# Optimization experiments

Hardware: AMD Instinct MI355X
Metric: run time of the kernel (lower is better)

Reference implementation:

```python
import jax, jax.numpy as jnp
import numpy as np

B, S, H, HD = 2, 2048, 16, 128
HID = H * HD            # 2048
FF = 4 * HID            # 8192
ROT = int(HD * 0.25)    # 32 rotary dims (rotary_pct=0.25)
EPS = 1e-5
ROPE_BASE = 10000.0


def _layernorm(x, g, b):
    mu = jnp.mean(x, axis=-1, keepdims=True)
    var = jnp.mean(jnp.square(x - mu), axis=-1, keepdims=True)
    return (x - mu) * jax.lax.rsqrt(var + EPS) * g + b


def _rope_cos_sin(seq_len, dim, dtype):
    inv_freq = 1.0 / (ROPE_BASE ** (np.arange(0, dim, 2, dtype=np.float32) / dim))
    t = np.arange(seq_len, dtype=np.float32)
    freqs = np.outer(t, inv_freq)              # [S, dim/2]
    emb = np.concatenate([freqs, freqs], -1)   # [S, dim]
    return jnp.asarray(np.cos(emb), dtype), jnp.asarray(np.sin(emb), dtype)


def _apply_rope(x, cos, sin):
    # x: [B, H, S, ROT]; GPTNeoX rotate_half
    half = x.shape[-1] // 2
    x1, x2 = x[..., :half], x[..., half:]
    rot = jnp.concatenate([-x2, x1], axis=-1)
    return x * cos[None, None, :, :] + rot * sin[None, None, :, :]


def setup_inputs() -> dict:
    key = jax.random.key(0)
    ks = jax.random.split(key, 8)
    f = jnp.float32
    return {
        "hidden_states": jax.random.normal(ks[0], (B, S, HID), f),
        "ln1_g": jnp.ones((HID,), f), "ln1_b": jnp.zeros((HID,), f),
        "ln2_g": jnp.ones((HID,), f), "ln2_b": jnp.zeros((HID,), f),
        "W_qkv": jax.random.normal(ks[1], (HID, 3 * HID), f) * 0.02,
        "b_qkv": jnp.zeros((3 * HID,), f),
        "W_o": jax.random.normal(ks[2], (HID, HID), f) * 0.02,
        "b_o": jnp.zeros((HID,), f),
        "W_fc": jax.random.normal(ks[3], (HID, FF), f) * 0.02,
        "b_fc": jnp.zeros((FF,), f),
        "W_proj": jax.random.normal(ks[4], (FF, HID), f) * 0.02,
        "b_proj": jnp.zeros((HID,), f),
    }


def reference(hidden_states, ln1_g, ln1_b, ln2_g, ln2_b,
              W_qkv, b_qkv, W_o, b_o, W_fc, b_fc, W_proj, b_proj):
    dtype = hidden_states.dtype
    x = _layernorm(hidden_states, ln1_g, ln1_b)

    # fused QKV, GPTNeoX per-head interleaved layout [B,S,H,3*HD]
    qkv = (x @ W_qkv + b_qkv).reshape(B, S, H, 3 * HD)
    q = jnp.transpose(qkv[..., :HD], (0, 2, 1, 3))          # [B,H,S,HD]
    k = jnp.transpose(qkv[..., HD:2 * HD], (0, 2, 1, 3))
    v = jnp.transpose(qkv[..., 2 * HD:], (0, 2, 1, 3))

    cos, sin = _rope_cos_sin(S, ROT, dtype)
    q = jnp.concatenate([_apply_rope(q[..., :ROT], cos, sin), q[..., ROT:]], -1)
    k = jnp.concatenate([_apply_rope(k[..., :ROT], cos, sin), k[..., ROT:]], -1)

    # eager attention: scores / sqrt(hd), causal mask-fill, softmax, matmul
    scale = 1.0 / jnp.sqrt(jnp.asarray(HD, dtype))
    scores = jnp.einsum("bhqd,bhkd->bhqk", q, k) * scale
    causal = jnp.tril(jnp.ones((S, S), bool))
    scores = jnp.where(causal, scores, jnp.finfo(dtype).min)
    weights = jax.nn.softmax(scores, axis=-1)
    ctx = jnp.einsum("bhqk,bhkd->bhqd", weights, v)          # [B,H,S,HD]
    ctx = jnp.transpose(ctx, (0, 2, 1, 3)).reshape(B, S, HID)
    attn_out = ctx @ W_o + b_o

    # parallel residual: mlp(ln2(h)) + attn(ln1(h)) + h
    m = _layernorm(hidden_states, ln2_g, ln2_b)
    mlp_out = jax.nn.gelu(m @ W_fc + b_fc, approximate=False) @ W_proj + b_proj
    return mlp_out + attn_out + hidden_states
```

## Files before the change

kernel.cpp:

```cpp
#include <hip/hip_runtime.h>
#include <hip/hip_bf16.h>
#include <math.h>

#define BDIM 2
#define SDIM 2048
#define HDIM 16
#define HD 128
#define HID 2048
#define FFD 8192
#define NTOK (BDIM*SDIM)
#define QKVW (3*HID)

typedef __hip_bfloat16 bf16;
typedef __attribute__((ext_vector_type(8))) short short8;
typedef __attribute__((ext_vector_type(4))) short short4_;
typedef __attribute__((ext_vector_type(4))) float floatx4;

__device__ inline short bfbits(float f) {
  bf16 h = __float2bfloat16(f);
  short s;
  __builtin_memcpy(&s, &h, 2);
  return s;
}

__device__ inline float fast_erf(float x) {
  float ax = fabsf(x);
  float t = __builtin_amdgcn_rcpf(1.0f + 0.3275911f * ax);
  float p = t * (0.254829592f + t * (-0.284496736f + t * (1.421413741f
          + t * (-1.453152027f + t * 1.061405429f))));
  float e = __expf(-ax * ax);
  float r = 1.0f - p * e;
  return copysignf(r, x);
}

__global__ __launch_bounds__(256) void transpose_cvt(
    const float* __restrict__ W, bf16* __restrict__ Wt, int K, int N)
{
  __shared__ float tile[32][33];
  int n0 = blockIdx.x * 32, k0 = blockIdx.y * 32;
  int tx = threadIdx.x, ty = threadIdx.y;
  #pragma unroll
  for (int r = ty; r < 32; r += 8)
    tile[r][tx] = W[(size_t)(k0 + r) * N + n0 + tx];
  __syncthreads();
  #pragma unroll
  for (int r = ty; r < 32; r += 8)
    Wt[(size_t)(n0 + r) * K + k0 + tx] = __float2bfloat16(tile[tx][r]);
}

__global__ __launch_bounds__(256) void ln_both(
    const float* __restrict__ x,
    const float* __restrict__ g1, const float* __restrict__ b1,
    const float* __restrict__ g2, const float* __restrict__ b2,
    bf16* __restrict__ o1, bf16* __restrict__ o2)
{
  int row = blockIdx.x;
  int tid = threadIdx.x;
  const float4* xr = (const float4*)(x + (size_t)row * HID);
  float4 va = xr[tid], vb = xr[tid + 256];
  float s = va.x + va.y + va.z + va.w + vb.x + vb.y + vb.z + vb.w;
  float q = va.x*va.x + va.y*va.y + va.z*va.z + va.w*va.w
          + vb.x*vb.x + vb.y*vb.y + vb.z*vb.z + vb.w*vb.w;
  #pragma unroll
  for (int off = 1; off < 64; off <<= 1) {
    s += __shfl_xor(s, off);
    q += __shfl_xor(q, off);
  }
  __shared__ float red[8];
  int wave = tid >> 6;
  if ((tid & 63) == 0) { red[wave] = s; red[4 + wave] = q; }
  __syncthreads();
  s = red[0] + red[1] + red[2] + red[3];
  q = red[4] + red[5] + red[6] + red[7];
  float mu = s * (1.0f / HID);
  float var = q * (1.0f / HID) - mu * mu;
  float rs = rsqrtf(var + 1e-5f);

  const float4* g1v = (const float4*)g1; const float4* b1v = (const float4*)b1;
  const float4* g2v = (const float4*)g2; const float4* b2v = (const float4*)b2;
  short4_* o1v = (short4_*)(o1 + (size_t)row * HID);
  short4_* o2v = (short4_*)(o2 + (size_t)row * HID);
  #pragma unroll
  for (int p = 0; p < 2; ++p) {
    int e = tid + p * 256;
    float4 xv = (p == 0) ? va : vb;
    float4 gv = g1v[e], bv = b1v[e];
    short4_ pk;
    pk[0] = bfbits((xv.x - mu) * rs * gv.x + bv.x);
    pk[1] = bfbits((xv.y - mu) * rs * gv.y + bv.y);
    pk[2] = bfbits((xv.z - mu) * rs * gv.z + bv.z);
    pk[3] = bfbits((xv.w - mu) * rs * gv.w + bv.w);
    o1v[e] = pk;
    gv = g2v[e]; bv = b2v[e];
    pk[0] = bfbits((xv.x - mu) * rs * gv.x + bv.x);
    pk[1] = bfbits((xv.y - mu) * rs * gv.y + bv.y);
    pk[2] = bfbits((xv.z - mu) * rs * gv.z + bv.z);
    pk[3] = bfbits((xv.w - mu) * rs * gv.w + bv.w);
    o2v[e] = pk;
  }
}

template<int EPI>
__global__ __launch_bounds__(256) void gemm_bt(
    const bf16* __restrict__ A, const bf16* __restrict__ Bt,
    const float* __restrict__ bias,
    float* __restrict__ Cf, bf16* __restrict__ Cb,
    const bf16* __restrict__ r1b, const float* __restrict__ r2,
    int M, int N, int K)
{
  __shared__ bf16 As[128 * 32];
  __shared__ bf16 Bs[128 * 32];
  const int tid = threadIdx.x;
  const int wave = tid >> 6, lane = tid & 63;
  const int quad = lane >> 4, l16 = lane & 15;

  const int nwg = gridDim.x * gridDim.y;
  const int flat = blockIdx.y * gridDim.x + blockIdx.x;
  const int swz = (flat & 7) * (nwg >> 3) + (flat >> 3);
  const int bx = swz % gridDim.x, by = swz / gridDim.x;
  const int n0 = bx * 128, m0 = by * 128;

  const int wm = (wave >> 1) * 64, wn = (wave & 1) * 64;
  const int lrow = lane >> 2, lcol = (lane & 3) * 8;

  floatx4 acc[4][4];
  #pragma unroll
  for (int i = 0; i < 4; ++i)
    #pragma unroll
    for (int j = 0; j < 4; ++j) acc[i][j] = (floatx4)0.0f;

  const int KT = K >> 5;
  for (int kt = 0; kt < KT; ++kt) {
    #pragma unroll
    for (int t = 0; t < 2; ++t) {
      int c = wave * 2 + t;
      const bf16* ga = A + (size_t)(m0 + c * 16 + lrow) * K + kt * 32 + lcol;
      const bf16* gb = Bt + (size_t)(n0 + c * 16 + lrow) * K + kt * 32 + lcol;
      __builtin_amdgcn_global_load_lds(
          (const __attribute__((address_space(1))) void*)ga,
          (__attribute__((address_space(3))) void*)&As[c * 512], 16, 0, 0);
      __builtin_amdgcn_global_load_lds(
          (const __attribute__((address_space(1))) void*)gb,
          (__attribute__((address_space(3))) void*)&Bs[c * 512], 16, 0, 0);
    }
    __syncthreads();
    short8 av[4], bv[4];
    #pragma unroll
    for (int i = 0; i < 4; ++i)
      av[i] = *(const short8*)&As[(wm + i * 16 + l16) * 32 + quad * 8];
    #pragma unroll
    for (int j = 0; j < 4; ++j)
      bv[j] = *(const short8*)&Bs[(wn + j * 16 + l16) * 32 + quad * 8];
    #pragma unroll
    for (int i = 0; i < 4; ++i)
      #pragma unroll
      for (int j = 0; j < 4; ++j)
        acc[i][j] = __builtin_amdgcn_mfma_f32_16x16x32_bf16(av[i], bv[j], acc[i][j], 0, 0, 0);
    __syncthreads();
  }

  #pragma unroll
  for (int i = 0; i < 4; ++i) {
    #pragma unroll
    for (int j = 0; j < 4; ++j) {
      int col = n0 + wn + j * 16 + l16;
      float bsv = bias[col];
      #pragma unroll
      for (int r = 0; r < 4; ++r) {
        int row = m0 + wm + i * 16 + quad * 4 + r;
        size_t idx = (size_t)row * N + col;
        float v = acc[i][j][r] + bsv;
        if (EPI == 1) {
          v = 0.5f * v * (1.0f + fast_erf(v * 0.70710678118654752f));
          Cb[idx] = __float2bfloat16(v);
        } else if (EPI == 2) {
          Cf[idx] = v + __bfloat162float(r1b[idx]) + r2[idx];
        } else {
          Cb[idx] = __float2bfloat16(v);
        }
      }
    }
  }
}

__global__ __launch_bounds__(256) void rope_vt(
    bf16* __restrict__ qkv, bf16* __restrict__ vT)
{
  int bh = blockIdx.x, s0 = blockIdx.y * 32;
  int b = bh >> 4, h = bh & 15;
  int tid = threadIdx.x;
  __shared__ bf16 vs[32][136];
  const float qsc = 0.12751740f;

  for (int idx = tid; idx < 512; idx += 256) {
    int sl = idx >> 4, d = idx & 15;
    int s = s0 + sl;
    bf16* base = qkv + (size_t)(b * SDIM + s) * QKVW + h * 384;
    float fr = (float)s * expf(-(float)d * 0.5756462732485114f);
    float c = cosf(fr), sn = sinf(fr);
    float q1 = __bfloat162float(base[d]);
    float q2 = __bfloat162float(base[d + 16]);
    float k1 = __bfloat162float(base[128 + d]);
    float k2 = __bfloat162float(base[128 + d + 16]);
    base[d]        = __float2bfloat16(qsc * (q1 * c - q2 * sn));
    base[d + 16]   = __float2bfloat16(qsc * (q2 * c + q1 * sn));
    base[128 + d]      = __float2bfloat16(k1 * c - k2 * sn);
    base[128 + d + 16] = __float2bfloat16(k2 * c + k1 * sn);
  }
  for (int idx = tid; idx < 32 * 96; idx += 256) {
    int sl = idx / 96, d = 32 + idx % 96;
    bf16* base = qkv + (size_t)(b * SDIM + s0 + sl) * QKVW + h * 384;
    base[d] = __float2bfloat16(qsc * __bfloat162float(base[d]));
  }

  for (int idx = tid; idx < 32 * 128; idx += 256) {
    int sl = idx >> 7, d = idx & 127;
    vs[sl][d] = qkv[(size_t)(b * SDIM + s0 + sl) * QKVW + h * 384 + 256 + d];
  }
  __syncthreads();
  for (int idx = tid; idx < 32 * 128; idx += 256) {
    int d = idx >> 5, sl = idx & 31;
    vT[((size_t)bh * HD + d) * SDIM + s0 + sl] = vs[sl][d];
  }
}

#define LOAD_K(KB, K0) { \
  int krow_ = (K0); \
  _Pragma("unroll") for (int nh_ = 0; nh_ < 2; ++nh_) \
    _Pragma("unroll") for (int c_ = 0; c_ < 4; ++c_) \
      KB[nh_*4+c_] = *(const short8*)&Kb[(size_t)(krow_ + nh_*16 + l16) * QKVW + c_*32 + quad*8]; }

#define SOFTMAX(S0, S1, MR, LR, OO, ROWQ, DOMASK, K0, SLOT) { \
  if (DOMASK) { \
    _Pragma("unroll") for (int r_ = 0; r_ < 4; ++r_) { \
      int row_ = (ROWQ) + quad*4 + r_; \
      S0[r_] = ((K0) + l16 <= row_) ? S0[r_] : -1e30f; \
      S1[r_] = ((K0) + 16 + l16 <= row_) ? S1[r_] : -1e30f; } } \
  _Pragma("unroll") for (int r_ = 0; r_ < 4; ++r_) { \
    float mx_ = fmaxf(S0[r_], S1[r_]); \
    mx_ = fmaxf(mx_, __shfl_xor(mx_, 1)); \
    mx_ = fmaxf(mx_, __shfl_xor(mx_, 2)); \
    mx_ = fmaxf(mx_, __shfl_xor(mx_, 4)); \
    mx_ = fmaxf(mx_, __shfl_xor(mx_, 8)); \
    float mnew_ = fmaxf(MR[r_], mx_); \
    float alpha_ = __builtin_amdgcn_exp2f(MR[r_] - mnew_); \
    MR[r_] = mnew_; \
    S0[r_] = __builtin_amdgcn_exp2f(S0[r_] - mnew_); \
    S1[r_] = __builtin_amdgcn_exp2f(S1[r_] - mnew_); \
    float sm_ = S0[r_] + S1[r_]; \
    sm_ += __shfl_xor(sm_, 1); sm_ += __shfl_xor(sm_, 2); \
    sm_ += __shfl_xor(sm_, 4); sm_ += __shfl_xor(sm_, 8); \
    LR[r_] = LR[r_] * alpha_ + sm_; \
    _Pragma("unroll") for (int d_ = 0; d_ < 8; ++d_) OO[d_][r_] *= alpha_; \
    Ps[wave][SLOT][quad*4 + r_][l16]      = __float2bfloat16(S0[r_]); \
    Ps[wave][SLOT][quad*4 + r_][16 + l16] = __float2bfloat16(S1[r_]); } }

#define FLASH_ITER(IT, KC, KN) { \
  const int k0_ = (IT) * 32; \
  const int k0n_ = ((IT) + 1 < nk) ? k0_ + 32 : 0; \
  LOAD_K(KN, k0n_); \
  short8 vbuf_[8]; \
  _Pragma("unroll") for (int d_ = 0; d_ < 8; ++d_) \
    vbuf_[d_] = *(const short8*)&Vb[(size_t)(d_*16 + l16) * SDIM + k0_ + quad*8]; \
  floatx4 scB_[2]; scB_[0] = (floatx4)0.0f; scB_[1] = (floatx4)0.0f; \
  _Pragma("unroll") for (int c_ = 0; c_ < 4; ++c_) { \
    scB_[0] = __builtin_amdgcn_mfma_f32_16x16x32_bf16(aqB[c_], KC[c_],   scB_[0], 0,0,0); \
    scB_[1] = __builtin_amdgcn_mfma_f32_16x16x32_bf16(aqB[c_], KC[4+c_], scB_[1], 0,0,0); } \
  const bool actA_ = (k0_ <= qa + 15); \
  floatx4 scA_[2]; scA_[0] = (floatx4)0.0f; scA_[1] = (floatx4)0.0f; \
  if (actA_) { \
    _Pragma("unroll") for (int c_ = 0; c_ < 4; ++c_) { \
      scA_[0] = __builtin_amdgcn_mfma_f32_16x16x32_bf16(aqA[c_], KC[c_],   scA_[0], 0,0,0); \
      scA_[1] = __builtin_amdgcn_mfma_f32_16x16x32_bf16(aqA[c_], KC[4+c_], scA_[1], 0,0,0); } } \
  SOFTMAX(scB_[0], scB_[1], mB, lB, oB, qb, (k0_ + 32 >= kmax), k0_, 0); \
  if (actA_) { \
    SOFTMAX(scA_[0], scA_[1], mA, lA, oA, qa, (k0_ + 32 > qa + 15), k0_, 1); \
    short8 pfB_ = *(const short8*)&Ps[wave][0][l16][quad*8]; \
    short8 pfA_ = *(const short8*)&Ps[wave][1][l16][quad*8]; \
    _Pragma("unroll") for (int d_ = 0; d_ < 8; ++d_) { \
      oB[d_] = __builtin_amdgcn_mfma_f32_16x16x32_bf16(pfB_, vbuf_[d_], oB[d_], 0,0,0); \
      oA[d_] = __builtin_amdgcn_mfma_f32_16x16x32_bf16(pfA_, vbuf_[d_], oA[d_], 0,0,0); } \
  } else { \
    short8 pfB_ = *(const short8*)&Ps[wave][0][l16][quad*8]; \
    _Pragma("unroll") for (int d_ = 0; d_ < 8; ++d_) \
      oB[d_] = __builtin_amdgcn_mfma_f32_16x16x32_bf16(pfB_, vbuf_[d_], oB[d_], 0,0,0); } }

__global__ __launch_bounds__(256) void flash_attn(
    const bf16* __restrict__ qkv, const bf16* __restrict__ vT,
    bf16* __restrict__ ctx)
{
  int bh = blockIdx.x;
  int b = bh >> 4, h = bh & 15;
  int tid = threadIdx.x;
  int wave = tid >> 6, lane = tid & 63;
  int quad = lane >> 4, l16 = lane & 15;
  int p = blockIdx.y * 4 + wave;
  int qa = 16 * p;
  int qb = SDIM - 16 * (p + 1);
  int kmax = qb + 16;
  int nk = (kmax + 31) >> 5;
  const bf16* Qb = qkv + (size_t)b * SDIM * QKVW + h * 384;
  const bf16* Kb = Qb + 128;
  const bf16* Vb = vT + (size_t)bh * HD * SDIM;
  __shared__ bf16 Ps[4][2][16][32];

  short8 aqA[4], aqB[4];
  #pragma unroll
  for (int c = 0; c < 4; ++c) {
    aqA[c] = *(const short8*)&Qb[(size_t)(qa + l16) * QKVW + c * 32 + quad * 8];
    aqB[c] = *(const short8*)&Qb[(size_t)(qb + l16) * QKVW + c * 32 + quad * 8];
  }

  floatx4 oA[8], oB[8];
  #pragma unroll
  for (int d = 0; d < 8; ++d) { oA[d] = (floatx4)0.0f; oB[d] = (floatx4)0.0f; }
  float mA[4] = {-INFINITY, -INFINITY, -INFINITY, -INFINITY};
  float mB[4] = {-INFINITY, -INFINITY, -INFINITY, -INFINITY};
  float lA[4] = {0.0f, 0.0f, 0.0f, 0.0f};
  float lB[4] = {0.0f, 0.0f, 0.0f, 0.0f};

  short8 kb0[8], kb1[8];
  LOAD_K(kb0, 0);
  for (int it = 0; it < nk; it += 2) {
    FLASH_ITER(it, kb0, kb1);
    if (it + 1 < nk) { FLASH_ITER(it + 1, kb1, kb0); }
  }

  float rlA[4], rlB[4];
  #pragma unroll
  for (int r = 0; r < 4; ++r) { rlA[r] = 1.0f / lA[r]; rlB[r] = 1.0f / lB[r]; }
  #pragma unroll
  for (int d = 0; d < 8; ++d) {
    #pragma unroll
    for (int r = 0; r < 4; ++r) {
      int rowA = qa + quad * 4 + r;
      int rowB = qb + quad * 4 + r;
      ctx[((size_t)b * SDIM + rowA) * HID + h * HD + d * 16 + l16] =
          __float2bfloat16(oA[d][r] * rlA[r]);
      ctx[((size_t)b * SDIM + rowB) * HID + h * HD + d * 16 + l16] =
          __float2bfloat16(oB[d][r] * rlB[r]);
    }
  }
}

extern "C" void kernel_launch(void* const* d_in, const int* in_sizes, int n_in,
                              void* d_out, int out_size, void* d_ws, size_t ws_size,
                              hipStream_t stream) {
  const float* hidden = (const float*)d_in[0];
  const float* ln1g = (const float*)d_in[1];
  const float* ln1b = (const float*)d_in[2];
  const float* ln2g = (const float*)d_in[3];
  const float* ln2b = (const float*)d_in[4];
  const float* Wqkv = (const float*)d_in[5];
  const float* bqkv = (const float*)d_in[6];
  const float* Wo   = (const float*)d_in[7];
  const float* bo   = (const float*)d_in[8];
  const float* Wfc  = (const float*)d_in[9];
  const float* bfc  = (const float*)d_in[10];
  const float* Wproj= (const float*)d_in[11];
  const float* bproj= (const float*)d_in[12];

  char* ws = (char*)d_ws;
  const size_t SZ_WQKV = (size_t)QKVW * HID * 2;
  const size_t SZ_WO   = (size_t)HID * HID * 2;
  const size_t SZ_WFC  = (size_t)FFD * HID * 2;
  const size_t SZ_WPROJ= (size_t)HID * FFD * 2;
  const size_t SZ_ACT  = (size_t)NTOK * HID * 2;
  const size_t SZ_QKV  = (size_t)NTOK * QKVW * 2;

  bf16* wqkvT = (bf16*)(ws + 0);
  bf16* woT   = (bf16*)(ws + SZ_WQKV);
  bf16* wfcT  = (bf16*)(ws + SZ_WQKV + SZ_WO);
  bf16* wprojT= (bf16*)(ws + SZ_WQKV + SZ_WO + SZ_WFC);
  char* actbase = ws + SZ_WQKV + SZ_WO + SZ_WFC + SZ_WPROJ;
  bf16* xln   = (bf16*)(actbase);
  bf16* mln   = (bf16*)(actbase + SZ_ACT);
  bf16* qkvb  = (bf16*)(actbase + 2 * SZ_ACT);
  bf16* vT    = (bf16*)(actbase + 2 * SZ_ACT + SZ_QKV);
  bf16* ctx   = xln;
  bf16* attnb = wqkvT;
  bf16* hfc   = qkvb;

  dim3 tblk(32, 8);
  transpose_cvt<<<dim3(QKVW / 32, HID / 32), tblk, 0, stream>>>(Wqkv, wqkvT, HID, QKVW);
  transpose_cvt<<<dim3(HID / 32, HID / 32), tblk, 0, stream>>>(Wo, woT, HID, HID);
  transpose_cvt<<<dim3(FFD / 32, HID / 32), tblk, 0, stream>>>(Wfc, wfcT, HID, FFD);
  transpose_cvt<<<dim3(HID / 32, FFD / 32), tblk, 0, stream>>>(Wproj, wprojT, FFD, HID);

  ln_both<<<NTOK, 256, 0, stream>>>(hidden, ln1g, ln1b, ln2g, ln2b, xln, mln);

  gemm_bt<3><<<dim3(48, 32), 256, 0, stream>>>(xln, wqkvT, bqkv, nullptr, qkvb,
                                               nullptr, nullptr, NTOK, QKVW, HID);

  rope_vt<<<dim3(32, SDIM / 32), 256, 0, stream>>>(qkvb, vT);

  flash_attn<<<dim3(32, SDIM / 128), 256, 0, stream>>>(qkvb, vT, ctx);

  gemm_bt<3><<<dim3(16, 32), 256, 0, stream>>>(ctx, woT, bo, nullptr, attnb,
                                               nullptr, nullptr, NTOK, HID, HID);

  gemm_bt<1><<<dim3(64, 32), 256, 0, stream>>>(mln, wfcT, bfc, nullptr, hfc,
                                               nullptr, nullptr, NTOK, FFD, HID);

  gemm_bt<2><<<dim3(16, 32), 256, 0, stream>>>(hfc, wprojT, bproj, (float*)d_out, nullptr,
                                               attnb, hidden, NTOK, HID, FFD);
}
```

Before: 1.131 ms.

## Add dedicated 256x256 double-buffered GEMM kernel for the GELU FC layer

```diff
diff --git a/kernel.cpp b/kernel.cpp
--- a/kernel.cpp
+++ b/kernel.cpp
@@ -113,13 +113,7 @@
   const int tid = threadIdx.x;
   const int wave = tid >> 6, lane = tid & 63;
   const int quad = lane >> 4, l16 = lane & 15;
-
-  const int nwg = gridDim.x * gridDim.y;
-  const int flat = blockIdx.y * gridDim.x + blockIdx.x;
-  const int swz = (flat & 7) * (nwg >> 3) + (flat >> 3);
-  const int bx = swz % gridDim.x, by = swz / gridDim.x;
-  const int n0 = bx * 128, m0 = by * 128;
-
+  const int n0 = blockIdx.x * 128, m0 = blockIdx.y * 128;
   const int wm = (wave >> 1) * 64, wn = (wave & 1) * 64;
   const int lrow = lane >> 2, lcol = (lane & 3) * 8;
 
@@ -170,14 +164,94 @@
         int row = m0 + wm + i * 16 + quad * 4 + r;
         size_t idx = (size_t)row * N + col;
         float v = acc[i][j][r] + bsv;
-        if (EPI == 1) {
-          v = 0.5f * v * (1.0f + fast_erf(v * 0.70710678118654752f));
-          Cb[idx] = __float2bfloat16(v);
-        } else if (EPI == 2) {
+        if (EPI == 2) {
           Cf[idx] = v + __bfloat162float(r1b[idx]) + r2[idx];
         } else {
           Cb[idx] = __float2bfloat16(v);
         }
+      }
+    }
+  }
+}
+
+__global__ __launch_bounds__(512, 2) void gemm_fc(
+    const bf16* __restrict__ A, const bf16* __restrict__ Bt,
+    const float* __restrict__ bias, bf16* __restrict__ Cb,
+    int M, int N, int K)
+{
+  __shared__ bf16 SA[2][256 * 64];
+  __shared__ bf16 SB[2][256 * 64];
+  const int tid = threadIdx.x;
+  const int wave = tid >> 6, lane = tid & 63;
+  const int quad = lane >> 4, l16 = lane & 15;
+  const int wr = wave >> 2, wc = wave & 3;
+  const int n0 = blockIdx.x * 256, m0 = blockIdx.y * 256;
+
+  const int stg_r = tid >> 3;
+  const int stg_c = ((tid & 7) ^ ((tid >> 3) & 7)) << 3;
+  const bf16* stgA = A + (size_t)(m0 + stg_r) * K + stg_c;
+  const bf16* stgB = Bt + (size_t)(n0 + stg_r) * K + stg_c;
+
+  floatx4 acc[8][4];
+  #pragma unroll
+  for (int i = 0; i < 8; ++i)
+    #pragma unroll
+    for (int j = 0; j < 4; ++j) acc[i][j] = (floatx4)0.0f;
+
+  const int KT = K >> 6;
+
+#define STAGE_FC(KT1, BUF) {                                                   \
+  const bf16* ga_ = stgA + (size_t)(KT1) * 64;                                 \
+  const bf16* gb_ = stgB + (size_t)(KT1) * 64;                                 \
+  _Pragma("unroll")                                                            \
+  for (int s_ = 0; s_ < 4; ++s_) {                                             \
+    __builtin_amdgcn_global_load_lds(                                          \
+        (const __attribute__((address_space(1))) void*)(ga_ + (size_t)s_ * 64 * K), \
+        (__attribute__((address_space(3))) void*)&SA[BUF][s_ * 4096 + wave * 512], 16, 0, 0); \
+    __builtin_amdgcn_global_load_lds(                                          \
+        (const __attribute__((address_space(1))) void*)(gb_ + (size_t)s_ * 64 * K), \
+        (__attribute__((address_space(3))) void*)&SB[BUF][s_ * 4096 + wave * 512], 16, 0, 0); } }
+
+  STAGE_FC(0, 0);
+  __syncthreads();
+
+  for (int kt = 0; kt < KT; ++kt) {
+    const int cur = kt & 1;
+    if (kt + 1 < KT) STAGE_FC(kt + 1, cur ^ 1);
+    const bf16* as_ = &SA[cur][0];
+    const bf16* bs_ = &SB[cur][0];
+    #pragma unroll
+    for (int kc = 0; kc < 2; ++kc) {
+      const int csw = (((kc * 4 + quad) ^ (l16 & 7)) << 3);
+      short8 av[8], bv[4];
+      #pragma unroll
+      for (int i = 0; i < 8; ++i)
+        av[i] = *(const short8*)&as_[(wr * 128 + i * 16 + l16) * 64 + csw];
+      #pragma unroll
+      for (int j = 0; j < 4; ++j)
+        bv[j] = *(const short8*)&bs_[(wc * 64 + j * 16 + l16) * 64 + csw];
+      #pragma unroll
+      for (int i = 0; i < 8; ++i)
+        #pragma unroll
+        for (int j = 0; j < 4; ++j)
+          acc[i][j] = __builtin_amdgcn_mfma_f32_16x16x32_bf16(av[i], bv[j], acc[i][j], 0, 0, 0);
+    }
+    __syncthreads();
+  }
+#undef STAGE_FC
+
+  #pragma unroll
+  for (int i = 0; i < 8; ++i) {
+    #pragma unroll
+    for (int j = 0; j < 4; ++j) {
+      int col = n0 + wc * 64 + j * 16 + l16;
+      float bsv = bias[col];
+      #pragma unroll
+      for (int r = 0; r < 4; ++r) {
+        int row = m0 + wr * 128 + i * 16 + quad * 4 + r;
+        float v = acc[i][j][r] + bsv;
+        v = 0.5f * v * (1.0f + fast_erf(v * 0.70710678118654752f));
+        Cb[(size_t)row * N + col] = __float2bfloat16(v);
       }
     }
   }
@@ -399,8 +473,8 @@
   gemm_bt<3><<<dim3(16, 32), 256, 0, stream>>>(ctx, woT, bo, nullptr, attnb,
                                                nullptr, nullptr, NTOK, HID, HID);
 
-  gemm_bt<1><<<dim3(64, 32), 256, 0, stream>>>(mln, wfcT, bfc, nullptr, hfc,
-                                               nullptr, nullptr, NTOK, FFD, HID);
+  gemm_fc<<<dim3(FFD / 256, NTOK / 256), 512, 0, stream>>>(
+      mln, wfcT, bfc, hfc, NTOK, FFD, HID);
 
   gemm_bt<2><<<dim3(16, 32), 256, 0, stream>>>(hfc, wprojT, bproj, (float*)d_out, nullptr,
                                                attnb, hidden, NTOK, HID, FFD);
```

Measured after the change: 1.049 ms. 7.3% less time.

## Replace GEMM with double-buffered 512-thread kernel using larger swizzled LDS tiles

Applied to the files above, without the earlier changes.

```diff
diff --git a/kernel.cpp b/kernel.cpp
--- a/kernel.cpp
+++ b/kernel.cpp
@@ -100,74 +100,87 @@
   }
 }
 
-template<int EPI>
-__global__ __launch_bounds__(256) void gemm_bt(
+template<int EPI, int BM>
+__global__ __launch_bounds__(512, 2) void gemm2p(
     const bf16* __restrict__ A, const bf16* __restrict__ Bt,
     const float* __restrict__ bias,
     float* __restrict__ Cf, bf16* __restrict__ Cb,
     const bf16* __restrict__ r1b, const float* __restrict__ r2,
     int M, int N, int K)
 {
-  __shared__ bf16 As[128 * 32];
-  __shared__ bf16 Bs[128 * 32];
+  constexpr int NI = BM / 32;
+  __shared__ bf16 SA[2][BM * 64];
+  __shared__ bf16 SB[2][256 * 64];
   const int tid = threadIdx.x;
   const int wave = tid >> 6, lane = tid & 63;
   const int quad = lane >> 4, l16 = lane & 15;
-
-  const int nwg = gridDim.x * gridDim.y;
-  const int flat = blockIdx.y * gridDim.x + blockIdx.x;
-  const int swz = (flat & 7) * (nwg >> 3) + (flat >> 3);
-  const int bx = swz % gridDim.x, by = swz / gridDim.x;
-  const int n0 = bx * 128, m0 = by * 128;
-
-  const int wm = (wave >> 1) * 64, wn = (wave & 1) * 64;
-  const int lrow = lane >> 2, lcol = (lane & 3) * 8;
-
-  floatx4 acc[4][4];
-  #pragma unroll
-  for (int i = 0; i < 4; ++i)
+  const int wr = wave >> 2, wc = wave & 3;
+  const int n0 = blockIdx.x * 256, m0 = blockIdx.y * BM;
+
+  const int stg_r = tid >> 3;
+  const int stg_c = ((tid & 7) ^ ((tid >> 3) & 7)) << 3;
+  const bf16* stgA = A + (size_t)(m0 + stg_r) * K + stg_c;
+  const bf16* stgB = Bt + (size_t)(n0 + stg_r) * K + stg_c;
+
+  floatx4 acc[NI][4];
+  #pragma unroll
+  for (int i = 0; i < NI; ++i)
     #pragma unroll
     for (int j = 0; j < 4; ++j) acc[i][j] = (floatx4)0.0f;
 
-  const int KT = K >> 5;
+  const int KT = K >> 6;
+
+#define STAGE_2P(KT1, BUF) {                                                   \
+  const bf16* ga_ = stgA + (size_t)(KT1) * 64;                                 \
+  const bf16* gb_ = stgB + (size_t)(KT1) * 64;                                 \
+  _Pragma("unroll")                                                            \
+  for (int s_ = 0; s_ < BM / 64; ++s_)                                         \
+    __builtin_amdgcn_global_load_lds(                                          \
+        (const __attribute__((address_space(1))) void*)(ga_ + (size_t)s_ * 64 * K), \
+        (__attribute__((address_space(3))) void*)&SA[BUF][s_ * 4096 + wave * 512], 16, 0, 0); \
+  _Pragma("unroll")                                                            \
+  for (int s_ = 0; s_ < 4; ++s_)                                               \
+    __builtin_amdgcn_global_load_lds(                                          \
+        (const __attribute__((address_space(1))) void*)(gb_ + (size_t)s_ * 64 * K), \
+        (__attribute__((address_space(3))) void*)&SB[BUF][s_ * 4096 + wave * 512], 16, 0, 0); }
+
+  STAGE_2P(0, 0);
+  __syncthreads();
+
   for (int kt = 0; kt < KT; ++kt) {
+    const int cur = kt & 1;
+    if (kt + 1 < KT) STAGE_2P(kt + 1, cur ^ 1);
+    const bf16* as_ = &SA[cur][0];
+    const bf16* bs_ = &SB[cur][0];
     #pragma unroll
-    for (int t = 0; t < 2; ++t) {
-      int c = wave * 2 + t;
-      const bf16* ga = A + (size_t)(m0 + c * 16 + lrow) * K + kt * 32 + lcol;
-      const bf16* gb = Bt + (size_t)(n0 + c * 16 + lrow) * K + kt * 32 + lcol;
-      __builtin_amdgcn_global_load_lds(
-          (const __attribute__((address_space(1))) void*)ga,
-          (__attribute__((address_space(3))) void*)&As[c * 512], 16, 0, 0);
-      __builtin_amdgcn_global_load_lds(
-          (const __attribute__((address_space(1))) void*)gb,
-          (__attribute__((address_space(3))) void*)&Bs[c * 512], 16, 0, 0);
+    for (int kc = 0; kc < 2; ++kc) {
+      const int csw = (((kc * 4 + quad) ^ (l16 & 7)) << 3);
+      short8 av[NI], bv[4];
+      #pragma unroll
+      for (int i = 0; i < NI; ++i)
+        av[i] = *(const short8*)&as_[(wr * (BM / 2) + i * 16 + l16) * 64 + csw];
+      #pragma unroll
+      for (int j = 0; j < 4; ++j)
+        bv[j] = *(const short8*)&bs_[(wc * 64 + j * 16 + l16) * 64 + csw];
+      #pragma unroll
+      for (int i = 0; i < NI; ++i)
+        #pragma unroll
+        for (int j = 0; j < 4; ++j)
+          acc[i][j] = __builtin_amdgcn_mfma_f32_16x16x32_bf16(av[i], bv[j], acc[i][j], 0, 0, 0);
     }
     __syncthreads();
-    short8 av[4], bv[4];
-    #pragma unroll
-    for (int i = 0; i < 4; ++i)
-      av[i] = *(const short8*)&As[(wm + i * 16 + l16) * 32 + quad * 8];
-    #pragma unroll
-    for (int j = 0; j < 4; ++j)
-      bv[j] = *(const short8*)&Bs[(wn + j * 16 + l16) * 32 + quad * 8];
-    #pragma unroll
-    for (int i = 0; i < 4; ++i)
-      #pragma unroll
-      for (int j = 0; j < 4; ++j)
-        acc[i][j] = __builtin_amdgcn_mfma_f32_16x16x32_bf16(av[i], bv[j], acc[i][j], 0, 0, 0);
-    __syncthreads();
-  }
-
-  #pragma unroll
-  for (int i = 0; i < 4; ++i) {
+  }
+#undef STAGE_2P
+
+  #pragma unroll
+  for (int i = 0; i < NI; ++i) {
     #pragma unroll
     for (int j = 0; j < 4; ++j) {
-      int col = n0 + wn + j * 16 + l16;
+      int col = n0 + wc * 64 + j * 16 + l16;
       float bsv = bias[col];
       #pragma unroll
       for (int r = 0; r < 4; ++r) {
-        int row = m0 + wm + i * 16 + quad * 4 + r;
+        int row = m0 + wr * (BM / 2) + i * 16 + quad * 4 + r;
         size_t idx = (size_t)row * N + col;
         float v = acc[i][j][r] + bsv;
         if (EPI == 1) {
@@ -389,19 +402,19 @@
 
   ln_both<<<NTOK, 256, 0, stream>>>(hidden, ln1g, ln1b, ln2g, ln2b, xln, mln);
 
-  gemm_bt<3><<<dim3(48, 32), 256, 0, stream>>>(xln, wqkvT, bqkv, nullptr, qkvb,
-                                               nullptr, nullptr, NTOK, QKVW, HID);
+  gemm2p<3, 128><<<dim3(QKVW / 256, NTOK / 128), 512, 0, stream>>>(
+      xln, wqkvT, bqkv, nullptr, qkvb, nullptr, nullptr, NTOK, QKVW, HID);
 
   rope_vt<<<dim3(32, SDIM / 32), 256, 0, stream>>>(qkvb, vT);
 
   flash_attn<<<dim3(32, SDIM / 128), 256, 0, stream>>>(qkvb, vT, ctx);
 
-  gemm_bt<3><<<dim3(16, 32), 256, 0, stream>>>(ctx, woT, bo, nullptr, attnb,
-                                               nullptr, nullptr, NTOK, HID, HID);
-
-  gemm_bt<1><<<dim3(64, 32), 256, 0, stream>>>(mln, wfcT, bfc, nullptr, hfc,
-                                               nullptr, nullptr, NTOK, FFD, HID);
-
-  gemm_bt<2><<<dim3(16, 32), 256, 0, stream>>>(hfc, wprojT, bproj, (float*)d_out, nullptr,
-                                               attnb, hidden, NTOK, HID, FFD);
-}
+  gemm2p<3, 128><<<dim3(HID / 256, NTOK / 128), 512, 0, stream>>>(
+      ctx, woT, bo, nullptr, attnb, nullptr, nullptr, NTOK, HID, HID);
+
+  gemm2p<1, 256><<<dim3(FFD / 256, NTOK / 256), 512, 0, stream>>>(
+      mln, wfcT, bfc, nullptr, hfc, nullptr, nullptr, NTOK, FFD, HID);
+
+  gemm2p<2, 128><<<dim3(HID / 256, NTOK / 128), 512, 0, stream>>>(
+      hfc, wprojT, bproj, (float*)d_out, nullptr, attnb, hidden, NTOK, HID, FFD);
+}
```

After: 1.036 ms. -8.4%, faster.
